# Kernel optimization log

Measured on AMD Instinct MI355X. Metric: run time of the kernel, lower is better.

## Reference

```python
import jax, jax.numpy as jnp
import numpy as np

EMBED = 1024
HEADS = 16
HEAD_DIM = EMBED // HEADS


def setup_inputs() -> dict:
    key = jax.random.key(0)
    ks = jax.random.split(key, 9)
    s = 0.02
    x = jax.random.normal(ks[0], (2, 2048, EMBED), dtype=jnp.float32)
    Wq = jax.random.normal(ks[1], (EMBED, EMBED), dtype=jnp.float32) * s
    bq = jnp.zeros((EMBED,), dtype=jnp.float32)
    Wk = jax.random.normal(ks[2], (EMBED, EMBED), dtype=jnp.float32) * s
    bk = jnp.zeros((EMBED,), dtype=jnp.float32)
    Wv = jax.random.normal(ks[3], (EMBED, EMBED), dtype=jnp.float32) * s
    bv = jnp.zeros((EMBED,), dtype=jnp.float32)
    Wo = jax.random.normal(ks[4], (EMBED, EMBED), dtype=jnp.float32) * s
    bo = jnp.zeros((EMBED,), dtype=jnp.float32)
    return {"x": x, "Wq": Wq, "bq": bq, "Wk": Wk, "bk": bk,
            "Wv": Wv, "bv": bv, "Wo": Wo, "bo": bo}


def reference(x, Wq, bq, Wk, bk, Wv, bv, Wo, bo):
    B, S, E = x.shape
    H, D = HEADS, HEAD_DIM
    scale = jnp.sqrt(jnp.asarray(D, dtype=x.dtype))
    # projections (torch Linear: y = x @ W.T + b)
    q = (x @ Wq.T + bq).reshape(B, S, H, D).transpose(0, 2, 1, 3)  # [B,H,S,D]
    k = (x @ Wk.T + bk).reshape(B, S, H, D).transpose(0, 2, 1, 3)
    v = (x @ Wv.T + bv).reshape(B, S, H, D).transpose(0, 2, 1, 3)
    scores = jnp.einsum('bhqd,bhkd->bhqk', q, k) / scale  # [B,H,S,S]
    probs = jax.nn.softmax(scores, axis=-1)
    out = jnp.einsum('bhqk,bhkd->bhqd', probs, v)  # [B,H,S,D]
    out = out.transpose(0, 2, 1, 3).reshape(B, S, E)
    return out @ Wo.T + bo
```

## Files before the change

### kernel.cpp

```cpp
#include <hip/hip_runtime.h>
#include <cstddef>

#define EMBED 1024
#define HEADS 16
#define HDIM  64
#define BATCH 2
#define SEQ   2048
#define MTOT  (BATCH*SEQ)

typedef __attribute__((ext_vector_type(8)))  short short8;
typedef __attribute__((ext_vector_type(4)))  float f32x4;
typedef __attribute__((ext_vector_type(16))) float f32x16;

typedef __attribute__((address_space(1))) const unsigned int* gas_u32p;
typedef __attribute__((address_space(3))) unsigned int* las_u32p;

static __device__ __forceinline__ void gload_lds16(const void* g, void* l) {
    __builtin_amdgcn_global_load_lds((gas_u32p)g, (las_u32p)l, 16, 0, 0);
}

static __device__ __forceinline__ unsigned short f2bf(float x) {
    unsigned u = __builtin_bit_cast(unsigned, x);
    unsigned r = (u + 0x7FFFu + ((u >> 16) & 1u)) >> 16;
    return (unsigned short)r;
}

static __device__ __forceinline__ unsigned pk_bf16(float lo, float hi) {
    unsigned r;
    asm("v_cvt_pk_bf16_f32 %0, %1, %2" : "=v"(r) : "v"(lo), "v"(hi));
    return r;
}

static __device__ __forceinline__ void plane32_swap(unsigned &a, unsigned &b) {
    auto r = __builtin_amdgcn_permlane32_swap((int)a, (int)b, false, false);
    a = (unsigned)r[0];
    b = (unsigned)r[1];
}

static __device__ __forceinline__ f32x16 mfma32(short8 a, short8 b, f32x16 c) {
    return __builtin_amdgcn_mfma_f32_32x32x16_bf16(a, b, c, 0, 0, 0);
}

__global__ __launch_bounds__(256)
void conv_all(const float* __restrict__ x,
              const float* __restrict__ Wq, const float* __restrict__ Wk,
              const float* __restrict__ Wv, const float* __restrict__ Wo,
              unsigned short* __restrict__ xh, unsigned short* __restrict__ Wh)
{
    const size_t i = ((size_t)blockIdx.x * 256 + threadIdx.x) * 8;
    const size_t XTOT = (size_t)MTOT * EMBED;
    const float* src;
    unsigned short* dst;
    size_t off;
    if (i < XTOT) {
        src = x; dst = xh; off = i;
    } else {
        size_t j = i - XTOT;
        int sel = (int)(j >> 20);
        off = j & ((1u << 20) - 1);
        src = sel == 0 ? Wq : sel == 1 ? Wk : sel == 2 ? Wv : Wo;
        dst = Wh + ((size_t)sel << 20);
    }
    float4 a = *(const float4*)(src + off);
    float4 b = *(const float4*)(src + off + 4);
    unsigned short o[8] __attribute__((aligned(16)));
    o[0] = f2bf(a.x); o[1] = f2bf(a.y); o[2] = f2bf(a.z); o[3] = f2bf(a.w);
    o[4] = f2bf(b.x); o[5] = f2bf(b.y); o[6] = f2bf(b.z); o[7] = f2bf(b.w);
    *(uint4*)(dst + off) = *(const uint4*)o;
}

__global__ __launch_bounds__(256)
void gemm_qkv_bf16(const unsigned short* __restrict__ A,
                   const unsigned short* __restrict__ Wqh,
                   const unsigned short* __restrict__ Wkh,
                   const unsigned short* __restrict__ Wvh,
                   const float* __restrict__ bq,
                   const float* __restrict__ bk,
                   const float* __restrict__ bv,
                   unsigned short* __restrict__ Qb,
                   unsigned short* __restrict__ Kb,
                   unsigned short* __restrict__ Vt)
{
    __shared__ short As[128 * 64];
    __shared__ short Bs[128 * 64];

    const int tid  = threadIdx.x;
    const int lane = tid & 63;
    const int w    = tid >> 6;
    const int c    = lane & 15;
    const int g    = lane >> 4;
    const int wr   = w >> 1;
    const int wc   = w & 1;

    const int m0   = blockIdx.y * 128;
    const int bxn  = blockIdx.x;
    const int wsel = bxn >> 3;
    const int n0   = (bxn & 7) * 128;

    const unsigned short* W = (wsel == 0) ? Wqh : (wsel == 1) ? Wkh : Wvh;
    const float* bias       = (wsel == 0) ? bq  : (wsel == 1) ? bk  : bv;

    f32x4 acc[4][4] = {};

    for (int k0 = 0; k0 < EMBED; k0 += 64) {
        __syncthreads();
        #pragma unroll
        for (int i = 0; i < 4; ++i) {
            const int slot = w * 256 + i * 64 + lane;
            const int row  = slot >> 3;
            const int chs  = (slot & 7) ^ (row & 7);
            gload_lds16(A + (size_t)(m0 + row) * EMBED + k0 + chs * 8,
                        As + (size_t)(w * 256 + i * 64) * 8);
            gload_lds16(W + (size_t)(n0 + row) * EMBED + k0 + chs * 8,
                        Bs + (size_t)(w * 256 + i * 64) * 8);
        }
        __syncthreads();

        #pragma unroll
        for (int ks = 0; ks < 2; ++ks) {
            short8 af[4], bf[4];
            #pragma unroll
            for (int mi = 0; mi < 4; ++mi) {
                const int row = wr * 64 + mi * 16 + c;
                const int chn = (ks * 4 + g) ^ (row & 7);
                af[mi] = *(const short8*)&As[row * 64 + chn * 8];
            }
            #pragma unroll
            for (int ni = 0; ni < 4; ++ni) {
                const int row = wc * 64 + ni * 16 + c;
                const int chn = (ks * 4 + g) ^ (row & 7);
                bf[ni] = *(const short8*)&Bs[row * 64 + chn * 8];
            }
            #pragma unroll
            for (int mi = 0; mi < 4; ++mi)
                #pragma unroll
                for (int ni = 0; ni < 4; ++ni)
                    acc[mi][ni] = __builtin_amdgcn_mfma_f32_16x16x32_bf16(
                        af[mi], bf[ni], acc[mi][ni], 0, 0, 0);
        }
    }

    if (wsel == 2) {
        #pragma unroll
        for (int mi = 0; mi < 4; ++mi) {
            const int m  = m0 + wr * 64 + mi * 16 + g * 4;
            const int bb = m >> 11;
            const int ss = m & (SEQ - 1);
            #pragma unroll
            for (int ni = 0; ni < 4; ++ni) {
                const int col = n0 + wc * 64 + ni * 16 + c;
                const int hh = col >> 6, dd = col & 63;
                const float bi_ = bias[col];
                ushort4 o;
                o.x = f2bf(acc[mi][ni][0] + bi_);
                o.y = f2bf(acc[mi][ni][1] + bi_);
                o.z = f2bf(acc[mi][ni][2] + bi_);
                o.w = f2bf(acc[mi][ni][3] + bi_);
                *(ushort4*)&Vt[((size_t)((bb * HEADS + hh) * HDIM) + dd) * SEQ + ss] = o;
            }
        }
    } else {
        unsigned short* Out = (wsel == 0) ? Qb : Kb;
        const float oscale  = (wsel == 0) ? 0.180336880f : 1.0f;
        #pragma unroll
        for (int mi = 0; mi < 4; ++mi)
            #pragma unroll
            for (int r = 0; r < 4; ++r) {
                const int m = m0 + wr * 64 + mi * 16 + g * 4 + r;
                #pragma unroll
                for (int ni = 0; ni < 4; ++ni) {
                    const int col = n0 + wc * 64 + ni * 16 + c;
                    Out[(size_t)m * EMBED + col] =
                        f2bf((acc[mi][ni][r] + bias[col]) * oscale);
                }
            }
    }
}

__global__ __launch_bounds__(256)
void gemm_o_bf16(const unsigned short* __restrict__ A,
                 const unsigned short* __restrict__ Woh,
                 const float* __restrict__ bo,
                 float* __restrict__ C)
{
    __shared__ short As[128 * 32];
    __shared__ short Bs[128 * 32];

    const int tid  = threadIdx.x;
    const int lane = tid & 63;
    const int w    = tid >> 6;
    const int c    = lane & 15;
    const int g    = lane >> 4;
    const int wr   = w >> 1;
    const int wc   = w & 1;

    const int m0 = blockIdx.y * 128;
    const int n0 = blockIdx.x * 128;

    f32x4 acc[4][4] = {};

    for (int k0 = 0; k0 < EMBED; k0 += 32) {
        __syncthreads();
        #pragma unroll
        for (int i = 0; i < 2; ++i) {
            int s   = (w * 2 + i) * 64 + lane;
            int row = s >> 2;
            int k8  = (s & 3) * 8;
            gload_lds16(A + (size_t)(m0 + row) * EMBED + k0 + k8,
                        As + (size_t)(w * 2 + i) * 512);
            gload_lds16(Woh + (size_t)(n0 + row) * EMBED + k0 + k8,
                        Bs + (size_t)(w * 2 + i) * 512);
        }
        __syncthreads();

        short8 af[4], bf[4];
        #pragma unroll
        for (int mi = 0; mi < 4; ++mi)
            af[mi] = *(const short8*)&As[(wr * 64 + mi * 16 + c) * 32 + g * 8];
        #pragma unroll
        for (int ni = 0; ni < 4; ++ni)
            bf[ni] = *(const short8*)&Bs[(wc * 64 + ni * 16 + c) * 32 + g * 8];
        #pragma unroll
        for (int mi = 0; mi < 4; ++mi)
            #pragma unroll
            for (int ni = 0; ni < 4; ++ni)
                acc[mi][ni] = __builtin_amdgcn_mfma_f32_16x16x32_bf16(
                    af[mi], bf[ni], acc[mi][ni], 0, 0, 0);
    }

    #pragma unroll
    for (int mi = 0; mi < 4; ++mi)
        #pragma unroll
        for (int r = 0; r < 4; ++r) {
            const int m = m0 + wr * 64 + mi * 16 + g * 4 + r;
            #pragma unroll
            for (int ni = 0; ni < 4; ++ni) {
                const int col = n0 + wc * 64 + ni * 16 + c;
                C[(size_t)m * EMBED + col] = acc[mi][ni][r] + bo[col];
            }
        }
}

__global__ __launch_bounds__(512, 4)
void flash_attn_mfma5(const unsigned short* __restrict__ Qb,
                      const unsigned short* __restrict__ Kb,
                      const unsigned short* __restrict__ Vt,
                      unsigned short* __restrict__ O)
{
    __shared__ short KT[2][2][64 * 64];
    __shared__ short VT[2][2][64 * 64];

    const int tid  = threadIdx.x;
    const int lane = tid & 63;
    const int w    = tid >> 6;
    const int qt   = w & 3;
    const int half = w >> 2;
    const int l31  = lane & 31;
    const int hi   = lane >> 5;
    const int q0   = blockIdx.x * 128 + qt * 32;
    const int h    = blockIdx.y;
    const int b    = blockIdx.z;

    short8 qf[4];
    {
        const unsigned short* qrow =
            Qb + (size_t)(b * SEQ + q0 + l31) * EMBED + h * HDIM + hi * 8;
        #pragma unroll
        for (int kc = 0; kc < 4; ++kc)
            qf[kc] = *(const short8*)(qrow + kc * 16);
    }

    const int tb     = w >> 1;
    const int sthalf = tb >> 1;
    const int stV    = tb & 1;
    const int ssub   = w & 1;
    const int strow  = ssub * 32 + (lane >> 3);
    const int ch     = (lane & 7) ^ (strow & 7);
    const unsigned short* kS =
        Kb + (size_t)(b * SEQ + sthalf * (SEQ / 2) + strow) * EMBED + h * HDIM + ch * 8;
    const unsigned short* vS =
        Vt + ((size_t)((b * HEADS + h) * HDIM) + strow) * SEQ + sthalf * (SEQ / 2) + ch * 8;

    f32x16 acc[2] = {};
    float l_run = 0.f;

    #define STAGE(kt2, bb)                                                    \
        do {                                                                  \
            if (stV == 0) {                                                   \
                const unsigned short* src = kS + (size_t)(kt2) * 64 * EMBED;  \
                short* kd = &KT[sthalf][bb][ssub * 2048];                     \
                _Pragma("unroll")                                             \
                for (int it = 0; it < 4; ++it)                                \
                    gload_lds16(src + (size_t)it * 8 * EMBED, kd + it * 512); \
            } else {                                                          \
                const unsigned short* src = vS + (kt2) * 64;                  \
                short* vd = &VT[sthalf][bb][ssub * 2048];                     \
                _Pragma("unroll")                                             \
                for (int it = 0; it < 4; ++it)                                \
                    gload_lds16(src + (size_t)it * 8 * SEQ, vd + it * 512);   \
            }                                                                 \
        } while (0)

    STAGE(0, 0);
    __syncthreads();

    for (int kt = 0; kt < SEQ / 2 / 64; ++kt) {
        const int bi = kt & 1;
        if (kt < SEQ / 2 / 64 - 1) STAGE(kt + 1, bi ^ 1);

        const short* kb_ = &KT[half][bi][0];
        const short* vb_ = &VT[half][bi][0];

        f32x16 s[2] = {};
        __builtin_amdgcn_s_setprio(1);
        #pragma unroll
        for (int t = 0; t < 2; ++t) {
            const int row = t * 32 + l31;
            const int rm  = l31 & 7;
            #pragma unroll
            for (int kc = 0; kc < 4; ++kc) {
                short8 ka = *(const short8*)&kb_[row * 64 + (((2 * kc + hi) ^ rm) * 8)];
                s[t] = mfma32(ka, qf[kc], s[t]);
            }
        }
        __builtin_amdgcn_s_setprio(0);

        float rs = 0.f;
        #pragma unroll
        for (int t = 0; t < 2; ++t)
            #pragma unroll
            for (int r = 0; r < 16; ++r) {
                float pv = __builtin_amdgcn_exp2f(s[t][r]);
                s[t][r] = pv;
                rs += pv;
            }
        rs += __shfl_xor(rs, 32, 64);
        l_run += rs;

        short8 pf[2][2];
        #pragma unroll
        for (int t = 0; t < 2; ++t)
            #pragma unroll
            for (int kc = 0; kc < 2; ++kc) {
                unsigned A0 = pk_bf16(s[t][8 * kc + 0], s[t][8 * kc + 1]);
                unsigned A1 = pk_bf16(s[t][8 * kc + 2], s[t][8 * kc + 3]);
                unsigned B0 = pk_bf16(s[t][8 * kc + 4], s[t][8 * kc + 5]);
                unsigned B1 = pk_bf16(s[t][8 * kc + 6], s[t][8 * kc + 7]);
                plane32_swap(A0, B0);
                plane32_swap(A1, B1);
                uint4 fw = make_uint4(A0, A1, B0, B1);
                pf[t][kc] = __builtin_bit_cast(short8, fw);
            }

        __builtin_amdgcn_s_setprio(1);
        #pragma unroll
        for (int dt = 0; dt < 2; ++dt) {
            const int row = dt * 32 + l31;
            const int rm  = l31 & 7;
            #pragma unroll
            for (int t = 0; t < 2; ++t)
                #pragma unroll
                for (int kc = 0; kc < 2; ++kc) {
                    short8 vf = *(const short8*)
                        &vb_[row * 64 + (((4 * t + 2 * kc + hi) ^ rm) * 8)];
                    acc[dt] = mfma32(pf[t][kc], vf, acc[dt]);
                }
        }
        __builtin_amdgcn_s_setprio(0);

        __syncthreads();
    }
    #undef STAGE

    float* mrgf = (float*)&KT[0][0][0];
    float* mlbf = (float*)&VT[0][0][0];
    if (half == 1) {
        #pragma unroll
        for (int dt = 0; dt < 2; ++dt)
            #pragma unroll
            for (int r = 0; r < 16; ++r) {
                const int qr = (r & 3) + 8 * (r >> 2) + 4 * hi;
                mrgf[qt * 2048 + qr * 64 + dt * 32 + l31] = acc[dt][r];
            }
        if (lane < 32)
            mlbf[qt * 32 + lane] = l_run;
    }
    __syncthreads();
    if (half == 0) {
        const float lo  = mlbf[qt * 32 + l31];
        const float inv = 1.f / (l_run + lo);
        #pragma unroll
        for (int r = 0; r < 16; ++r) {
            const int qr = (r & 3) + 8 * (r >> 2) + 4 * hi;
            float invr = __shfl(inv, qr, 64);
            #pragma unroll
            for (int dt = 0; dt < 2; ++dt) {
                float oh  = mrgf[qt * 2048 + qr * 64 + dt * 32 + l31];
                float val = (acc[dt][r] + oh) * invr;
                O[(size_t)(b * SEQ + q0 + qr) * EMBED + h * HDIM + dt * 32 + l31]
                    = f2bf(val);
            }
        }
    }
}

extern "C" void kernel_launch(void* const* d_in, const int* in_sizes, int n_in,
                              void* d_out, int out_size, void* d_ws, size_t ws_size,
                              hipStream_t stream)
{
    const float* x  = (const float*)d_in[0];
    const float* Wq = (const float*)d_in[1];
    const float* bq = (const float*)d_in[2];
    const float* Wk = (const float*)d_in[3];
    const float* bk = (const float*)d_in[4];
    const float* Wv = (const float*)d_in[5];
    const float* bv = (const float*)d_in[6];
    const float* Wo = (const float*)d_in[7];
    const float* bo = (const float*)d_in[8];
    float* out = (float*)d_out;

    const size_t ME = (size_t)MTOT * EMBED;
    unsigned short* xh   = (unsigned short*)d_ws;
    unsigned short* Qb   = xh   + ME;
    unsigned short* Kb   = Qb   + ME;
    unsigned short* Vt   = Kb   + ME;
    unsigned short* attn = Vt   + ME;
    unsigned short* Wh   = attn + ME;

    dim3 blk(256);

    conv_all<<<dim3((2 * ME) / 2048), blk, 0, stream>>>(x, Wq, Wk, Wv, Wo, xh, Wh);

    gemm_qkv_bf16<<<dim3(24, MTOT / 128), blk, 0, stream>>>(
        xh, Wh, Wh + (size_t)EMBED * EMBED, Wh + 2 * (size_t)EMBED * EMBED,
        bq, bk, bv, Qb, Kb, Vt);

    flash_attn_mfma5<<<dim3(SEQ / 128, HEADS, BATCH), dim3(512), 0, stream>>>(
        Qb, Kb, Vt, attn);

    gemm_o_bf16<<<dim3(EMBED / 128, MTOT / 128), blk, 0, stream>>>(
        attn, Wh + 3 * (size_t)EMBED * EMBED, bo, out);
}
```

Measured before the change: 117.9 us.

## Double query rows per attention wave and widen O-proj K-tile with swizzled LDS

Result: slower. 123.7 us (+4.9%).

```diff
diff --git a/kernel.cpp b/kernel.cpp
--- a/kernel.cpp
+++ b/kernel.cpp
@@ -183,8 +183,8 @@
                  const float* __restrict__ bo,
                  float* __restrict__ C)
 {
-    __shared__ short As[128 * 32];
-    __shared__ short Bs[128 * 32];
+    __shared__ short As[128 * 64];
+    __shared__ short Bs[128 * 64];
 
     const int tid  = threadIdx.x;
     const int lane = tid & 63;
@@ -199,33 +199,42 @@
 
     f32x4 acc[4][4] = {};
 
-    for (int k0 = 0; k0 < EMBED; k0 += 32) {
+    for (int k0 = 0; k0 < EMBED; k0 += 64) {
         __syncthreads();
         #pragma unroll
-        for (int i = 0; i < 2; ++i) {
-            int s   = (w * 2 + i) * 64 + lane;
-            int row = s >> 2;
-            int k8  = (s & 3) * 8;
-            gload_lds16(A + (size_t)(m0 + row) * EMBED + k0 + k8,
-                        As + (size_t)(w * 2 + i) * 512);
-            gload_lds16(Woh + (size_t)(n0 + row) * EMBED + k0 + k8,
-                        Bs + (size_t)(w * 2 + i) * 512);
+        for (int i = 0; i < 4; ++i) {
+            const int slot = w * 256 + i * 64 + lane;
+            const int row  = slot >> 3;
+            const int chs  = (slot & 7) ^ (row & 7);
+            gload_lds16(A   + (size_t)(m0 + row) * EMBED + k0 + chs * 8,
+                        As + (size_t)(w * 256 + i * 64) * 8);
+            gload_lds16(Woh + (size_t)(n0 + row) * EMBED + k0 + chs * 8,
+                        Bs + (size_t)(w * 256 + i * 64) * 8);
         }
         __syncthreads();
 
-        short8 af[4], bf[4];
-        #pragma unroll
-        for (int mi = 0; mi < 4; ++mi)
-            af[mi] = *(const short8*)&As[(wr * 64 + mi * 16 + c) * 32 + g * 8];
-        #pragma unroll
-        for (int ni = 0; ni < 4; ++ni)
-            bf[ni] = *(const short8*)&Bs[(wc * 64 + ni * 16 + c) * 32 + g * 8];
-        #pragma unroll
-        for (int mi = 0; mi < 4; ++mi)
-            #pragma unroll
-            for (int ni = 0; ni < 4; ++ni)
-                acc[mi][ni] = __builtin_amdgcn_mfma_f32_16x16x32_bf16(
-                    af[mi], bf[ni], acc[mi][ni], 0, 0, 0);
+        #pragma unroll
+        for (int ks = 0; ks < 2; ++ks) {
+            short8 af[4], bf[4];
+            #pragma unroll
+            for (int mi = 0; mi < 4; ++mi) {
+                const int row = wr * 64 + mi * 16 + c;
+                const int chn = (ks * 4 + g) ^ (row & 7);
+                af[mi] = *(const short8*)&As[row * 64 + chn * 8];
+            }
+            #pragma unroll
+            for (int ni = 0; ni < 4; ++ni) {
+                const int row = wc * 64 + ni * 16 + c;
+                const int chn = (ks * 4 + g) ^ (row & 7);
+                bf[ni] = *(const short8*)&Bs[row * 64 + chn * 8];
+            }
+            #pragma unroll
+            for (int mi = 0; mi < 4; ++mi)
+                #pragma unroll
+                for (int ni = 0; ni < 4; ++ni)
+                    acc[mi][ni] = __builtin_amdgcn_mfma_f32_16x16x32_bf16(
+                        af[mi], bf[ni], acc[mi][ni], 0, 0, 0);
+        }
     }
 
     #pragma unroll
@@ -241,33 +250,35 @@
         }
 }
 
-__global__ __launch_bounds__(512, 4)
-void flash_attn_mfma5(const unsigned short* __restrict__ Qb,
+__global__ __launch_bounds__(512)
+void flash_attn_mfma6(const unsigned short* __restrict__ Qb,
                       const unsigned short* __restrict__ Kb,
                       const unsigned short* __restrict__ Vt,
                       unsigned short* __restrict__ O)
 {
-    __shared__ short KT[2][2][64 * 64];
-    __shared__ short VT[2][2][64 * 64];
+    __shared__ short SLDS[32768];
+    __shared__ float MLB[4][64];
 
     const int tid  = threadIdx.x;
     const int lane = tid & 63;
     const int w    = tid >> 6;
-    const int qt   = w & 3;
+    const int qp   = w & 3;
     const int half = w >> 2;
     const int l31  = lane & 31;
     const int hi   = lane >> 5;
-    const int q0   = blockIdx.x * 128 + qt * 32;
+    const int rm   = l31 & 7;
+    const int q0   = blockIdx.x * 256 + qp * 64;
     const int h    = blockIdx.y;
     const int b    = blockIdx.z;
 
-    short8 qf[4];
-    {
+    short8 qf[2][4];
+    #pragma unroll
+    for (int sub = 0; sub < 2; ++sub) {
         const unsigned short* qrow =
-            Qb + (size_t)(b * SEQ + q0 + l31) * EMBED + h * HDIM + hi * 8;
+            Qb + (size_t)(b * SEQ + q0 + sub * 32 + l31) * EMBED + h * HDIM + hi * 8;
         #pragma unroll
         for (int kc = 0; kc < 4; ++kc)
-            qf[kc] = *(const short8*)(qrow + kc * 16);
+            qf[sub][kc] = *(const short8*)(qrow + kc * 16);
     }
 
     const int tb     = w >> 1;
@@ -281,20 +292,21 @@
     const unsigned short* vS =
         Vt + ((size_t)((b * HEADS + h) * HDIM) + strow) * SEQ + sthalf * (SEQ / 2) + ch * 8;
 
-    f32x16 acc[2] = {};
-    float l_run = 0.f;
+    f32x16 acc[2][2] = {};
+    float l_run[2] = {0.f, 0.f};
 
     #define STAGE(kt2, bb)                                                    \
         do {                                                                  \
             if (stV == 0) {                                                   \
                 const unsigned short* src = kS + (size_t)(kt2) * 64 * EMBED;  \
-                short* kd = &KT[sthalf][bb][ssub * 2048];                     \
+                short* kd = &SLDS[(sthalf * 2 + (bb)) * 4096 + ssub * 2048];  \
                 _Pragma("unroll")                                             \
                 for (int it = 0; it < 4; ++it)                                \
                     gload_lds16(src + (size_t)it * 8 * EMBED, kd + it * 512); \
             } else {                                                          \
                 const unsigned short* src = vS + (kt2) * 64;                  \
-                short* vd = &VT[sthalf][bb][ssub * 2048];                     \
+                short* vd = &SLDS[16384 + (sthalf * 2 + (bb)) * 4096          \
+                                  + ssub * 2048];                            \
                 _Pragma("unroll")                                             \
                 for (int it = 0; it < 4; ++it)                                \
                     gload_lds16(src + (size_t)it * 8 * SEQ, vd + it * 512);   \
@@ -308,97 +320,112 @@
         const int bi = kt & 1;
         if (kt < SEQ / 2 / 64 - 1) STAGE(kt + 1, bi ^ 1);
 
-        const short* kb_ = &KT[half][bi][0];
-        const short* vb_ = &VT[half][bi][0];
-
-        f32x16 s[2] = {};
+        const short* kb_ = &SLDS[(half * 2 + bi) * 4096];
+        const short* vb_ = &SLDS[16384 + (half * 2 + bi) * 4096];
+
+        short8 ka[2][4];
+        #pragma unroll
+        for (int t = 0; t < 2; ++t)
+            #pragma unroll
+            for (int kc = 0; kc < 4; ++kc)
+                ka[t][kc] = *(const short8*)
+                    &kb_[(t * 32 + l31) * 64 + (((2 * kc + hi) ^ rm) * 8)];
+
+        short8 pf[2][2][2];
+        #pragma unroll
+        for (int sub = 0; sub < 2; ++sub) {
+            f32x16 s[2] = {};
+            __builtin_amdgcn_s_setprio(1);
+            #pragma unroll
+            for (int t = 0; t < 2; ++t)
+                #pragma unroll
+                for (int kc = 0; kc < 4; ++kc)
+                    s[t] = mfma32(ka[t][kc], qf[sub][kc], s[t]);
+            __builtin_amdgcn_s_setprio(0);
+
+            float rs = 0.f;
+            #pragma unroll
+            for (int t = 0; t < 2; ++t)
+                #pragma unroll
+                for (int r = 0; r < 16; ++r) {
+                    float pv = __builtin_amdgcn_exp2f(s[t][r]);
+                    s[t][r] = pv;
+                    rs += pv;
+                }
+            l_run[sub] += rs;
+
+            #pragma unroll
+            for (int t = 0; t < 2; ++t)
+                #pragma unroll
+                for (int kc = 0; kc < 2; ++kc) {
+                    unsigned A0 = pk_bf16(s[t][8 * kc + 0], s[t][8 * kc + 1]);
+                    unsigned A1 = pk_bf16(s[t][8 * kc + 2], s[t][8 * kc + 3]);
+                    unsigned B0 = pk_bf16(s[t][8 * kc + 4], s[t][8 * kc + 5]);
+                    unsigned B1 = pk_bf16(s[t][8 * kc + 6], s[t][8 * kc + 7]);
+                    plane32_swap(A0, B0);
+                    plane32_swap(A1, B1);
+                    uint4 fw = make_uint4(A0, A1, B0, B1);
+                    pf[sub][t][kc] = __builtin_bit_cast(short8, fw);
+                }
+        }
+
         __builtin_amdgcn_s_setprio(1);
         #pragma unroll
-        for (int t = 0; t < 2; ++t) {
-            const int row = t * 32 + l31;
-            const int rm  = l31 & 7;
-            #pragma unroll
-            for (int kc = 0; kc < 4; ++kc) {
-                short8 ka = *(const short8*)&kb_[row * 64 + (((2 * kc + hi) ^ rm) * 8)];
-                s[t] = mfma32(ka, qf[kc], s[t]);
-            }
-        }
-        __builtin_amdgcn_s_setprio(0);
-
-        float rs = 0.f;
-        #pragma unroll
-        for (int t = 0; t < 2; ++t)
-            #pragma unroll
-            for (int r = 0; r < 16; ++r) {
-                float pv = __builtin_amdgcn_exp2f(s[t][r]);
-                s[t][r] = pv;
-                rs += pv;
-            }
-        rs += __shfl_xor(rs, 32, 64);
-        l_run += rs;
-
-        short8 pf[2][2];
-        #pragma unroll
-        for (int t = 0; t < 2; ++t)
-            #pragma unroll
-            for (int kc = 0; kc < 2; ++kc) {
-                unsigned A0 = pk_bf16(s[t][8 * kc + 0], s[t][8 * kc + 1]);
-                unsigned A1 = pk_bf16(s[t][8 * kc + 2], s[t][8 * kc + 3]);
-                unsigned B0 = pk_bf16(s[t][8 * kc + 4], s[t][8 * kc + 5]);
-                unsigned B1 = pk_bf16(s[t][8 * kc + 6], s[t][8 * kc + 7]);
-                plane32_swap(A0, B0);
-                plane32_swap(A1, B1);
-                uint4 fw = make_uint4(A0, A1, B0, B1);
-                pf[t][kc] = __builtin_bit_cast(short8, fw);
-            }
-
-        __builtin_amdgcn_s_setprio(1);
-        #pragma unroll
-        for (int dt = 0; dt < 2; ++dt) {
-            const int row = dt * 32 + l31;
-            const int rm  = l31 & 7;
+        for (int dt = 0; dt < 2; ++dt)
             #pragma unroll
             for (int t = 0; t < 2; ++t)
                 #pragma unroll
                 for (int kc = 0; kc < 2; ++kc) {
                     short8 vf = *(const short8*)
-                        &vb_[row * 64 + (((4 * t + 2 * kc + hi) ^ rm) * 8)];
-                    acc[dt] = mfma32(pf[t][kc], vf, acc[dt]);
-                }
-        }
+                        &vb_[(dt * 32 + l31) * 64 + (((4 * t + 2 * kc + hi) ^ rm) * 8)];
+                    acc[0][dt] = mfma32(pf[0][t][kc], vf, acc[0][dt]);
+                    acc[1][dt] = mfma32(pf[1][t][kc], vf, acc[1][dt]);
+                }
         __builtin_amdgcn_s_setprio(0);
 
         __syncthreads();
     }
     #undef STAGE
 
-    float* mrgf = (float*)&KT[0][0][0];
-    float* mlbf = (float*)&VT[0][0][0];
+    float lt[2];
+    #pragma unroll
+    for (int sub = 0; sub < 2; ++sub)
+        lt[sub] = l_run[sub] + __shfl_xor(l_run[sub], 32, 64);
+
+    float* mrgf = (float*)&SLDS[0];
     if (half == 1) {
         #pragma unroll
-        for (int dt = 0; dt < 2; ++dt)
+        for (int sub = 0; sub < 2; ++sub)
+            #pragma unroll
+            for (int dt = 0; dt < 2; ++dt)
+                #pragma unroll
+                for (int r = 0; r < 16; ++r) {
+                    const int qr = (r & 3) + 8 * (r >> 2) + 4 * hi;
+                    mrgf[qp * 4096 + (sub * 32 + qr) * 64 + dt * 32 + l31]
+                        = acc[sub][dt][r];
+                }
+        if (hi == 0) {
+            MLB[qp][l31]      = lt[0];
+            MLB[qp][l31 + 32] = lt[1];
+        }
+    }
+    __syncthreads();
+    if (half == 0) {
+        #pragma unroll
+        for (int sub = 0; sub < 2; ++sub) {
+            const float lo  = MLB[qp][sub * 32 + l31];
+            const float inv = 1.f / (lt[sub] + lo);
             #pragma unroll
             for (int r = 0; r < 16; ++r) {
                 const int qr = (r & 3) + 8 * (r >> 2) + 4 * hi;
-                mrgf[qt * 2048 + qr * 64 + dt * 32 + l31] = acc[dt][r];
-            }
-        if (lane < 32)
-            mlbf[qt * 32 + lane] = l_run;
-    }
-    __syncthreads();
-    if (half == 0) {
-        const float lo  = mlbf[qt * 32 + l31];
-        const float inv = 1.f / (l_run + lo);
-        #pragma unroll
-        for (int r = 0; r < 16; ++r) {
-            const int qr = (r & 3) + 8 * (r >> 2) + 4 * hi;
-            float invr = __shfl(inv, qr, 64);
-            #pragma unroll
-            for (int dt = 0; dt < 2; ++dt) {
-                float oh  = mrgf[qt * 2048 + qr * 64 + dt * 32 + l31];
-                float val = (acc[dt][r] + oh) * invr;
-                O[(size_t)(b * SEQ + q0 + qr) * EMBED + h * HDIM + dt * 32 + l31]
-                    = f2bf(val);
+                float invr = __shfl(inv, qr, 64);
+                #pragma unroll
+                for (int dt = 0; dt < 2; ++dt) {
+                    float oh = mrgf[qp * 4096 + (sub * 32 + qr) * 64 + dt * 32 + l31];
+                    float val = (acc[sub][dt][r] + oh) * invr;
+                    O[(size_t)(b * SEQ + q0 + sub * 32 + qr) * EMBED
+                      + h * HDIM + dt * 32 + l31] = f2bf(val);
+                }
             }
         }
     }
@@ -435,7 +462,7 @@
         xh, Wh, Wh + (size_t)EMBED * EMBED, Wh + 2 * (size_t)EMBED * EMBED,
         bq, bk, bv, Qb, Kb, Vt);
 
-    flash_attn_mfma5<<<dim3(SEQ / 128, HEADS, BATCH), dim3(512), 0, stream>>>(
+    flash_attn_mfma6<<<dim3(SEQ / 256, HEADS, BATCH), dim3(512), 0, stream>>>(
         Qb, Kb, Vt, attn);
 
     gemm_o_bf16<<<dim3(EMBED / 128, MTOT / 128), blk, 0, stream>>>(
```
